# Kernel tuning notes

Hardware: AMD Instinct MI355X
Metric: run time of the kernel (lower is better)

## Reference

```python
import jax, jax.numpy as jnp
import numpy as np

B, D, H, L, T = 4096, 1024, 2048, 256, 8
STD = 0.02


def setup_inputs() -> dict:
    key = jax.random.key(0)
    ks = jax.random.split(key, 24)
    n = lambda k, shp: (jax.random.normal(k, shp, dtype=jnp.float32) * STD)
    inp = {
        "x": jax.random.uniform(ks[0], (B, D), dtype=jnp.float32),
        "task": jax.random.randint(ks[1], (B,), 0, T),
        "eps": jax.random.normal(ks[2], (B, L), dtype=jnp.float32),
        # per-task encoder stacks: in->H->H->H->2L
        "enc_W1": n(ks[3], (T, D, H)), "enc_b1": jnp.zeros((T, H)),
        "enc_W2": n(ks[4], (T, H, H)), "enc_b2": jnp.zeros((T, H)),
        "enc_W3": n(ks[5], (T, H, H)), "enc_b3": jnp.zeros((T, H)),
        "enc_W4": n(ks[6], (T, H, 2 * L)), "enc_b4": jnp.zeros((T, 2 * L)),
        # shared decoder (BayesianLinear means): L->H->H
        "ds_W1": n(ks[7], (L, H)), "ds_b1": jnp.zeros((H,)),
        "ds_W2": n(ks[8], (H, H)), "ds_b2": jnp.zeros((H,)),
        # per-task decoder heads: H->H->D with Sigmoid
        "hd_W1": n(ks[9], (T, H, H)), "hd_b1": jnp.zeros((T, H)),
        "hd_W2": n(ks[10], (T, H, D)), "hd_b2": jnp.zeros((T, D)),
    }
    return inp


def reference(x, task, eps,
              enc_W1, enc_b1, enc_W2, enc_b2, enc_W3, enc_b3, enc_W4, enc_b4,
              ds_W1, ds_b1, ds_W2, ds_b2,
              hd_W1, hd_b1, hd_W2, hd_b2):
    ntasks = enc_W1.shape[0]
    onehot = jax.nn.one_hot(task, ntasks, dtype=x.dtype)  # [B, T], the task==idx mask

    # ---- encode: run every task's encoder on the full batch, mask-sum ----
    def enc_one(W1, b1, W2, b2, W3, b3, W4, b4):
        h = jax.nn.relu(x @ W1 + b1)
        h = jax.nn.relu(h @ W2 + b2)
        h = jax.nn.relu(h @ W3 + b3)
        return h @ W4 + b4  # [B, 2L]

    enc_all = jax.vmap(enc_one)(enc_W1, enc_b1, enc_W2, enc_b2,
                                enc_W3, enc_b3, enc_W4, enc_b4)  # [T, B, 2L]
    scat = jnp.einsum('tbd,bt->bd', enc_all, onehot)  # [B, 2L]
    latent = scat.shape[1] // 2
    mu, log_sigma = scat[:, :latent], scat[:, latent:]
    z = mu + jnp.exp(log_sigma) * eps  # reparameterization

    # ---- decode: shared trunk, then every head masked ----
    h = jax.nn.relu(z @ ds_W1 + ds_b1)
    h = jax.nn.relu(h @ ds_W2 + ds_b2)  # [B, H]

    def head_one(W1, b1, W2, b2):
        g = jax.nn.relu(h @ W1 + b1)
        return jax.nn.sigmoid(g @ W2 + b2)  # [B, D]

    heads_all = jax.vmap(head_one)(hd_W1, hd_b1, hd_W2, hd_b2)  # [T, B, D]
    return jnp.einsum('tbd,bt->bd', heads_all, onehot)  # [B, D]
```

## Files before the change

kernel.cpp:

```cpp
#include <hip/hip_runtime.h>
#include <hip/hip_bf16.h>

#define T_TASKS 8
#define B_ROWS 4096
#define PADROWS 4224
#define BM 128
#define BN 64
#define BK 32
#define MAXTILES 40

typedef __attribute__((ext_vector_type(4))) float f32x4;
typedef __attribute__((ext_vector_type(8))) short bf16x8;

#define GLOAD_LDS16(g, l) __builtin_amdgcn_global_load_lds( \
    (const __attribute__((address_space(1))) void*)(g), \
    (__attribute__((address_space(3))) void*)(l), 16, 0, 0)

__device__ __forceinline__ unsigned short f32_to_bf16(float f) {
    union { float f; unsigned int u; } v; v.f = f;
    unsigned int r = v.u + 0x7FFF + ((v.u >> 16) & 1);
    return (unsigned short)(r >> 16);
}

__device__ __forceinline__ unsigned int pack2_bf16(float lo, float hi) {
    __hip_bfloat162 h = __float22bfloat162_rn(make_float2(lo, hi));
    union { __hip_bfloat162 h; unsigned int u; } c; c.h = h;
    return c.u;
}

__global__ void setup_kernel(const int* __restrict__ task, int* __restrict__ perm,
                             int* __restrict__ offs, int* __restrict__ table) {
    __shared__ int cnt[T_TASKS];
    __shared__ int cur[T_TASKS];
    int tid = threadIdx.x;
    if (tid < T_TASKS) cnt[tid] = 0;
    __syncthreads();
    for (int b = tid; b < B_ROWS; b += blockDim.x)
        atomicAdd(&cnt[task[b]], 1);
    __syncthreads();
    if (tid == 0) {
        int o = 0;
        for (int t = 0; t < T_TASKS; ++t) { offs[t] = o; cur[t] = o; o += cnt[t]; }
        offs[T_TASKS] = o;
        int s = 0;
        for (int t = 0; t < T_TASKS; ++t) {
            int nt = (cnt[t] + BM - 1) / BM;
            for (int j = 0; j < nt; ++j) table[s++] = (t << 16) | j;
        }
        for (; s < MAXTILES; ++s) table[s] = -1;
    }
    __syncthreads();
    for (int b = tid; b < B_ROWS; b += blockDim.x) {
        int t = task[b];
        int pos = atomicAdd(&cur[t], 1);
        perm[pos] = b;
    }
}

__global__ void permute_cast_kernel(const float* __restrict__ x, const int* __restrict__ perm,
                                    unsigned short* __restrict__ xp) {
    int rowp = blockIdx.x;
    int src = perm[rowp];
    const float4* xin = reinterpret_cast<const float4*>(x + (size_t)src * 1024);
    unsigned short* dst = xp + (size_t)rowp * 1024;
    int c4 = threadIdx.x;
    float4 v = xin[c4];
    ushort4 o;
    o.x = f32_to_bf16(v.x); o.y = f32_to_bf16(v.y);
    o.z = f32_to_bf16(v.z); o.w = f32_to_bf16(v.w);
    *reinterpret_cast<ushort4*>(dst + c4 * 4) = o;
}

__global__ void vae_kernel(const float* __restrict__ scat, const float* __restrict__ eps,
                           const int* __restrict__ perm, unsigned short* __restrict__ z) {
    int rowp = blockIdx.x;
    int c = threadIdx.x;
    int src = perm[rowp];
    float mu = scat[(size_t)rowp * 512 + c];
    float ls = scat[(size_t)rowp * 512 + 256 + c];
    float e  = eps[(size_t)src * 256 + c];
    z[(size_t)rowp * 256 + c] = f32_to_bf16(mu + __expf(ls) * e);
}

template<int MODE>
__global__ __launch_bounds__(256, 4)
void gemm8_kernel(const unsigned short* __restrict__ A,
                  const float* __restrict__ W,
                  const float* __restrict__ bias, void* __restrict__ dst,
                  const int* __restrict__ offs, const int* __restrict__ table,
                  const int* __restrict__ perm,
                  int K, int N, int ldd, int Btot, int GX)
{
    __shared__ unsigned short As[2][BM * BK];
    __shared__ unsigned short Bs[2][BN * BK];

    const int bxh = blockIdx.x;
    const int tid = threadIdx.x;

    int bx = (bxh & 7) * (GX >> 3) + (bxh >> 3);

    int t, mtile, off, cnt;
    if (table != nullptr) {
        int v = table[bx];
        if (v < 0) return;
        t = v >> 16; mtile = v & 0xFFFF;
        off = offs[t]; cnt = offs[t + 1] - off;
    } else {
        t = 0; mtile = bx; off = 0; cnt = Btot;
    }
    const int n0 = blockIdx.y * BN;

    const int lane = tid & 63;
    const int wave = tid >> 6;
    const int wr = wave >> 1, wc = wave & 1;

    const int rl   = lane >> 2;
    const int csrc = ((lane & 3) ^ ((rl >> 1) & 3)) * 8;
    const unsigned short* Ab = A + ((size_t)(off + mtile * BM + rl)) * K + csrc;

    const int bn = lane;
    const int bc = wave;
    const float* Wb = W + (size_t)t * K * N + n0 + bn;
    const int bslot = (bc ^ ((bn >> 1) & 3)) * 8;
    float br[8];

    auto stage_a = [&](int buf, int k0) {
        #pragma unroll
        for (int jj = 0; jj < 2; ++jj) {
            int j = wave * 2 + jj;
            GLOAD_LDS16(Ab + (size_t)(j * 16) * K + k0, &As[buf][j * 512]);
        }
    };
    auto load_b = [&](int k0) {
        const float* p = Wb + (size_t)(k0 + bc * 8) * N;
        #pragma unroll
        for (int j = 0; j < 8; ++j)
            br[j] = p[(size_t)j * N];
    };
    auto write_b = [&](int buf) {
        uint4 wv;
        wv.x = pack2_bf16(br[0], br[1]);
        wv.y = pack2_bf16(br[2], br[3]);
        wv.z = pack2_bf16(br[4], br[5]);
        wv.w = pack2_bf16(br[6], br[7]);
        *reinterpret_cast<uint4*>(&Bs[buf][bn * 32 + bslot]) = wv;
    };

    f32x4 acc[4][2];
    #pragma unroll
    for (int m = 0; m < 4; ++m)
        #pragma unroll
        for (int n = 0; n < 2; ++n)
            acc[m][n] = (f32x4){0.f, 0.f, 0.f, 0.f};

    auto compute = [&](int buf) {
        bf16x8 af[4], bfr[2];
        #pragma unroll
        for (int m = 0; m < 4; ++m) {
            int rf = wr * 64 + m * 16 + (lane & 15);
            af[m] = *reinterpret_cast<const bf16x8*>(
                &As[buf][rf * 32 + (((lane >> 4) ^ ((rf >> 1) & 3)) * 8)]);
        }
        #pragma unroll
        for (int n = 0; n < 2; ++n) {
            int nf = wc * 32 + n * 16 + (lane & 15);
            bfr[n] = *reinterpret_cast<const bf16x8*>(
                &Bs[buf][nf * 32 + (((lane >> 4) ^ ((nf >> 1) & 3)) * 8)]);
        }
        #pragma unroll
        for (int m = 0; m < 4; ++m)
            #pragma unroll
            for (int n = 0; n < 2; ++n)
                acc[m][n] = __builtin_amdgcn_mfma_f32_16x16x32_bf16(af[m], bfr[n], acc[m][n], 0, 0, 0);
    };

    const int nsteps = K / BK;
    load_b(0);
    stage_a(0, 0);
    write_b(0);
    __syncthreads();

    int cur = 0;
    for (int s = 0; s < nsteps; ++s) {
        if (s + 1 < nsteps) {
            load_b((s + 1) * BK);
            stage_a(cur ^ 1, (s + 1) * BK);
        }
        compute(cur);
        if (s + 1 < nsteps) write_b(cur ^ 1);
        __syncthreads();
        cur ^= 1;
    }

    const float* bt = bias + (size_t)t * N;
    #pragma unroll
    for (int n = 0; n < 2; ++n) {
        int col = n0 + wc * 32 + n * 16 + (lane & 15);
        float bv = bt[col];
        #pragma unroll
        for (int m = 0; m < 4; ++m) {
            int rbase = mtile * BM + wr * 64 + m * 16 + ((lane >> 4) << 2);
            #pragma unroll
            for (int j = 0; j < 4; ++j) {
                int local = rbase + j;
                if (local >= cnt) continue;
                float v = acc[m][n][j] + bv;
                if (MODE == 0) {
                    ((unsigned short*)dst)[(size_t)(off + local) * ldd + col] =
                        f32_to_bf16(fmaxf(v, 0.f));
                } else if (MODE == 1) {
                    ((float*)dst)[(size_t)(off + local) * ldd + col] = v;
                } else {
                    int grow = perm[off + local];
                    ((float*)dst)[(size_t)grow * ldd + col] = 1.f / (1.f + __expf(-v));
                }
            }
        }
    }
}

extern "C" void kernel_launch(void* const* d_in, const int* in_sizes, int n_in,
                              void* d_out, int out_size, void* d_ws, size_t ws_size,
                              hipStream_t stream) {
    const float* x      = (const float*)d_in[0];
    const int*   task   = (const int*)d_in[1];
    const float* eps    = (const float*)d_in[2];
    const float* enc_W1 = (const float*)d_in[3];
    const float* enc_b1 = (const float*)d_in[4];
    const float* enc_W2 = (const float*)d_in[5];
    const float* enc_b2 = (const float*)d_in[6];
    const float* enc_W3 = (const float*)d_in[7];
    const float* enc_b3 = (const float*)d_in[8];
    const float* enc_W4 = (const float*)d_in[9];
    const float* enc_b4 = (const float*)d_in[10];
    const float* ds_W1  = (const float*)d_in[11];
    const float* ds_b1  = (const float*)d_in[12];
    const float* ds_W2  = (const float*)d_in[13];
    const float* ds_b2  = (const float*)d_in[14];
    const float* hd_W1  = (const float*)d_in[15];
    const float* hd_b1  = (const float*)d_in[16];
    const float* hd_W2  = (const float*)d_in[17];
    const float* hd_b2  = (const float*)d_in[18];
    float* out = (float*)d_out;

    char* ws = (char*)d_ws;
    int* perm  = (int*)ws;
    int* offs  = (int*)(ws + 16384);
    int* table = (int*)(ws + 16384 + 256);
    char* p = ws + 32768;
    unsigned short* xp = (unsigned short*)p; p += (size_t)PADROWS * 1024 * 2;
    unsigned short* h1 = (unsigned short*)p; p += (size_t)PADROWS * 2048 * 2;
    unsigned short* h2 = (unsigned short*)p; p += (size_t)PADROWS * 2048 * 2;
    unsigned short* zb = (unsigned short*)p; p += (size_t)PADROWS * 256 * 2;
    float* scat = out;

    setup_kernel<<<1, 1024, 0, stream>>>(task, perm, offs, table);
    permute_cast_kernel<<<B_ROWS, 256, 0, stream>>>(x, perm, xp);

    gemm8_kernel<0><<<dim3(MAXTILES, 32), 256, 0, stream>>>(xp, enc_W1, enc_b1, h1, offs, table, nullptr, 1024, 2048, 2048, B_ROWS, MAXTILES);
    gemm8_kernel<0><<<dim3(MAXTILES, 32), 256, 0, stream>>>(h1, enc_W2, enc_b2, h2, offs, table, nullptr, 2048, 2048, 2048, B_ROWS, MAXTILES);
    gemm8_kernel<0><<<dim3(MAXTILES, 32), 256, 0, stream>>>(h2, enc_W3, enc_b3, h1, offs, table, nullptr, 2048, 2048, 2048, B_ROWS, MAXTILES);
    gemm8_kernel<1><<<dim3(MAXTILES, 8), 256, 0, stream>>>(h1, enc_W4, enc_b4, scat, offs, table, nullptr, 2048, 512, 512, B_ROWS, MAXTILES);

    vae_kernel<<<B_ROWS, 256, 0, stream>>>(scat, eps, perm, zb);

    gemm8_kernel<0><<<dim3(32, 32), 256, 0, stream>>>(zb, ds_W1, ds_b1, h2, nullptr, nullptr, nullptr, 256, 2048, 2048, B_ROWS, 32);
    gemm8_kernel<0><<<dim3(32, 32), 256, 0, stream>>>(h2, ds_W2, ds_b2, h1, nullptr, nullptr, nullptr, 2048, 2048, 2048, B_ROWS, 32);

    gemm8_kernel<0><<<dim3(MAXTILES, 32), 256, 0, stream>>>(h1, hd_W1, hd_b1, h2, offs, table, nullptr, 2048, 2048, 2048, B_ROWS, MAXTILES);
    gemm8_kernel<2><<<dim3(MAXTILES, 16), 256, 0, stream>>>(h2, hd_W2, hd_b2, out, offs, table, perm, 2048, 1024, 1024, B_ROWS, MAXTILES);
}
```

Measured before the change: 664.6 us.

## Triple-buffer GEMM main loop with two-deep prefetch and partial vmcnt waits

The GEMM moves from double- to triple-buffered LDS tiles for A and B and prefetches two K-steps ahead, with two register sets alternating for the fp32 weight loads. A plain __syncthreads is replaced by an explicit s_waitcnt vmcnt(10) plus s_barrier, so the in-flight loads for later stages can stay outstanding while the current tile is computed. This is meant to hide global memory latency better behind the MFMA work. In exchange it uses more LDS and registers, which may lower occupancy. Out-of-range prefetches are clamped to the last K tile, and the loop is unrolled by two, which assumes an even step count.

```diff
diff --git a/kernel.cpp b/kernel.cpp
--- a/kernel.cpp
+++ b/kernel.cpp
@@ -15,6 +15,9 @@
 #define GLOAD_LDS16(g, l) __builtin_amdgcn_global_load_lds( \
     (const __attribute__((address_space(1))) void*)(g), \
     (__attribute__((address_space(3))) void*)(l), 16, 0, 0)
+
+#define WAITV10() asm volatile("s_waitcnt vmcnt(10)" ::: "memory")
+#define BAR() do { __builtin_amdgcn_s_barrier(); __builtin_amdgcn_sched_barrier(0); } while (0)
 
 __device__ __forceinline__ unsigned short f32_to_bf16(float f) {
     union { float f; unsigned int u; } v; v.f = f;
@@ -84,15 +87,15 @@
 
 template<int MODE>
 __global__ __launch_bounds__(256, 4)
-void gemm8_kernel(const unsigned short* __restrict__ A,
+void gemm9_kernel(const unsigned short* __restrict__ A,
                   const float* __restrict__ W,
                   const float* __restrict__ bias, void* __restrict__ dst,
                   const int* __restrict__ offs, const int* __restrict__ table,
                   const int* __restrict__ perm,
                   int K, int N, int ldd, int Btot, int GX)
 {
-    __shared__ unsigned short As[2][BM * BK];
-    __shared__ unsigned short Bs[2][BN * BK];
+    __shared__ unsigned short As[3][BM * BK];
+    __shared__ unsigned short Bs[3][BN * BK];
 
     const int bxh = blockIdx.x;
     const int tid = threadIdx.x;
@@ -122,7 +125,11 @@
     const int bc = wave;
     const float* Wb = W + (size_t)t * K * N + n0 + bn;
     const int bslot = (bc ^ ((bn >> 1) & 3)) * 8;
-    float br[8];
+    float brA[8], brB[8];
+
+    const int nsteps = K / BK;
+    const int kmax = K - BK;
+    auto kc = [&](int s) { int k = s * BK; return k > kmax ? kmax : k; };
 
     auto stage_a = [&](int buf, int k0) {
         #pragma unroll
@@ -131,13 +138,13 @@
             GLOAD_LDS16(Ab + (size_t)(j * 16) * K + k0, &As[buf][j * 512]);
         }
     };
-    auto load_b = [&](int k0) {
+    auto load_b = [&](float (&br)[8], int k0) {
         const float* p = Wb + (size_t)(k0 + bc * 8) * N;
         #pragma unroll
         for (int j = 0; j < 8; ++j)
             br[j] = p[(size_t)j * N];
     };
-    auto write_b = [&](int buf) {
+    auto write_b = [&](int buf, float (&br)[8]) {
         uint4 wv;
         wv.x = pack2_bf16(br[0], br[1]);
         wv.y = pack2_bf16(br[2], br[3]);
@@ -174,22 +181,24 @@
                 acc[m][n] = __builtin_amdgcn_mfma_f32_16x16x32_bf16(af[m], bfr[n], acc[m][n], 0, 0, 0);
     };
 
-    const int nsteps = K / BK;
-    load_b(0);
-    stage_a(0, 0);
-    write_b(0);
-    __syncthreads();
-
-    int cur = 0;
-    for (int s = 0; s < nsteps; ++s) {
-        if (s + 1 < nsteps) {
-            load_b((s + 1) * BK);
-            stage_a(cur ^ 1, (s + 1) * BK);
-        }
-        compute(cur);
-        if (s + 1 < nsteps) write_b(cur ^ 1);
-        __syncthreads();
-        cur ^= 1;
+    load_b(brA, kc(0));
+    stage_a(0, kc(0));
+    load_b(brB, kc(1));
+    stage_a(1, kc(1));
+    write_b(0, brA);
+    load_b(brA, kc(2));
+
+    for (int j = 0; j < nsteps; j += 2) {
+        WAITV10(); BAR();
+        compute(j % 3);
+        write_b((j + 1) % 3, brB);
+        load_b(brB, kc(j + 3));
+        stage_a((j + 2) % 3, kc(j + 2));
+        WAITV10(); BAR();
+        compute((j + 1) % 3);
+        write_b((j + 2) % 3, brA);
+        load_b(brA, kc(j + 4));
+        stage_a((j + 3) % 3, kc(j + 3));
     }
 
     const float* bt = bias + (size_t)t * N;
@@ -257,16 +266,16 @@
     setup_kernel<<<1, 1024, 0, stream>>>(task, perm, offs, table);
     permute_cast_kernel<<<B_ROWS, 256, 0, stream>>>(x, perm, xp);
 
-    gemm8_kernel<0><<<dim3(MAXTILES, 32), 256, 0, stream>>>(xp, enc_W1, enc_b1, h1, offs, table, nullptr, 1024, 2048, 2048, B_ROWS, MAXTILES);
-    gemm8_kernel<0><<<dim3(MAXTILES, 32), 256, 0, stream>>>(h1, enc_W2, enc_b2, h2, offs, table, nullptr, 2048, 2048, 2048, B_ROWS, MAXTILES);
-    gemm8_kernel<0><<<dim3(MAXTILES, 32), 256, 0, stream>>>(h2, enc_W3, enc_b3, h1, offs, table, nullptr, 2048, 2048, 2048, B_ROWS, MAXTILES);
-    gemm8_kernel<1><<<dim3(MAXTILES, 8), 256, 0, stream>>>(h1, enc_W4, enc_b4, scat, offs, table, nullptr, 2048, 512, 512, B_ROWS, MAXTILES);
+    gemm9_kernel<0><<<dim3(MAXTILES, 32), 256, 0, stream>>>(xp, enc_W1, enc_b1, h1, offs, table, nullptr, 1024, 2048, 2048, B_ROWS, MAXTILES);
+    gemm9_kernel<0><<<dim3(MAXTILES, 32), 256, 0, stream>>>(h1, enc_W2, enc_b2, h2, offs, table, nullptr, 2048, 2048, 2048, B_ROWS, MAXTILES);
+    gemm9_kernel<0><<<dim3(MAXTILES, 32), 256, 0, stream>>>(h2, enc_W3, enc_b3, h1, offs, table, nullptr, 2048, 2048, 2048, B_ROWS, MAXTILES);
+    gemm9_kernel<1><<<dim3(MAXTILES, 8), 256, 0, stream>>>(h1, enc_W4, enc_b4, scat, offs, table, nullptr, 2048, 512, 512, B_ROWS, MAXTILES);
 
     vae_kernel<<<B_ROWS, 256, 0, stream>>>(scat, eps, perm, zb);
 
-    gemm8_kernel<0><<<dim3(32, 32), 256, 0, stream>>>(zb, ds_W1, ds_b1, h2, nullptr, nullptr, nullptr, 256, 2048, 2048, B_ROWS, 32);
-    gemm8_kernel<0><<<dim3(32, 32), 256, 0, stream>>>(h2, ds_W2, ds_b2, h1, nullptr, nullptr, nullptr, 2048, 2048, 2048, B_ROWS, 32);
-
-    gemm8_kernel<0><<<dim3(MAXTILES, 32), 256, 0, stream>>>(h1, hd_W1, hd_b1, h2, offs, table, nullptr, 2048, 2048, 2048, B_ROWS, MAXTILES);
-    gemm8_kernel<2><<<dim3(MAXTILES, 16), 256, 0, stream>>>(h2, hd_W2, hd_b2, out, offs, table, perm, 2048, 1024, 1024, B_ROWS, MAXTILES);
-}
+    gemm9_kernel<0><<<dim3(32, 32), 256, 0, stream>>>(zb, ds_W1, ds_b1, h2, nullptr, nullptr, nullptr, 256, 2048, 2048, B_ROWS, 32);
+    gemm9_kernel<0><<<dim3(32, 32), 256, 0, stream>>>(h2, ds_W2, ds_b2, h1, nullptr, nullptr, nullptr, 2048, 2048, 2048, B_ROWS, 32);
+
+    gemm9_kernel<0><<<dim3(MAXTILES, 32), 256, 0, stream>>>(h1, hd_W1, hd_b1, h2, offs, table, nullptr, 2048, 2048, 2048, B_ROWS, MAXTILES);
+    gemm9_kernel<2><<<dim3(MAXTILES, 16), 256, 0, stream>>>(h2, hd_W2, hd_b2, out, offs, table, perm, 2048, 1024, 1024, B_ROWS, MAXTILES);
+}
```

Result: slower. 717.9 us (+8.0%).
